# Kernel tuning notes

Hardware: AMD Instinct MI355X
Metric: run time of the kernel (lower is better)

The kernel has to match this reference:

```python
import jax, jax.numpy as jnp
import numpy as np

N_NODES = 50000
N_EDGES = 800000
N_GRAPHS = 64
IN_DIM = 128
HID = 32
HEADS = 4
EDGE_DIM = 8
OUT = 10


def setup_inputs() -> dict:
    key = jax.random.key(0)
    ks = jax.random.split(key, 20)
    s = 0.1
    inp = {
        "x": jax.random.normal(ks[0], (N_NODES, IN_DIM), jnp.float32),
        "edge_index": jax.random.randint(ks[1], (2, N_EDGES), 0, N_NODES, jnp.int32),
        "edge_attr": jax.random.normal(ks[2], (N_EDGES, EDGE_DIM), jnp.float32),
        "batch": jnp.sort(jax.random.randint(ks[3], (N_NODES,), 0, N_GRAPHS, jnp.int32)),
        # conv1: heads=4, out=32
        "W1": jax.random.normal(ks[4], (IN_DIM, HEADS * HID), jnp.float32) * s,
        "att_src1": jax.random.normal(ks[5], (HEADS, HID), jnp.float32) * s,
        "att_dst1": jax.random.normal(ks[6], (HEADS, HID), jnp.float32) * s,
        "We1": jax.random.normal(ks[7], (EDGE_DIM, HEADS * HID), jnp.float32) * s,
        "att_e1": jax.random.normal(ks[8], (HEADS, HID), jnp.float32) * s,
        "b1": jnp.zeros((HEADS * HID,), jnp.float32),
        # conv2: heads=1, out=32
        "W2": jax.random.normal(ks[9], (HEADS * HID, HID), jnp.float32) * s,
        "att_src2": jax.random.normal(ks[10], (1, HID), jnp.float32) * s,
        "att_dst2": jax.random.normal(ks[11], (1, HID), jnp.float32) * s,
        "We2": jax.random.normal(ks[12], (EDGE_DIM, HID), jnp.float32) * s,
        "att_e2": jax.random.normal(ks[13], (1, HID), jnp.float32) * s,
        "b2": jnp.zeros((HID,), jnp.float32),
        # MLP head
        "W3": jax.random.normal(ks[14], (HID, HID // 2), jnp.float32) * s,
        "b3": jnp.zeros((HID // 2,), jnp.float32),
        "W4": jax.random.normal(ks[15], (HID // 2, OUT), jnp.float32) * s,
        "b4": jnp.zeros((OUT,), jnp.float32),
    }
    return inp


def _gat_conv(x, src, dst, eattr, W, a_s, a_d, We, a_e, b, H, C, N):
    """PyG GATConv math (self-loops already appended to src/dst/eattr)."""
    h = (x @ W).reshape(-1, H, C)            # [N,H,C]
    e = (eattr @ We).reshape(-1, H, C)       # [E,H,C]
    al_s = jnp.sum(h * a_s, -1)              # [N,H]
    al_d = jnp.sum(h * a_d, -1)              # [N,H]
    alpha = al_s[src] + al_d[dst] + jnp.sum(e * a_e, -1)   # [E,H]
    alpha = jax.nn.leaky_relu(alpha, 0.2)
    # segment softmax over incoming edges of each dst node
    m = jax.ops.segment_max(alpha, dst, num_segments=N)
    ealpha = jnp.exp(alpha - m[dst])
    denom = jax.ops.segment_sum(ealpha, dst, num_segments=N)
    ealpha = ealpha / (denom[dst] + 1e-16)
    msg = h[src] * ealpha[:, :, None]        # [E,H,C]
    out = jax.ops.segment_sum(msg, dst, num_segments=N)  # [N,H,C]
    return out.reshape(N, H * C) + b


def _forward(x, edge_index, edge_attr, batch,
             W1, att_src1, att_dst1, We1, att_e1, b1,
             W2, att_src2, att_dst2, We2, att_e2, b2,
             W3, b3, W4, b4):
    N = x.shape[0]
    src, dst = edge_index[0], edge_index[1]
    # add_self_loops with fill_value='mean': loop attr = mean of incoming edge_attr
    cnt = jax.ops.segment_sum(jnp.ones((src.shape[0],), x.dtype), dst, num_segments=N)
    loop_attr = jax.ops.segment_sum(edge_attr, dst, num_segments=N) / jnp.maximum(cnt, 1.0)[:, None]
    ar = jnp.arange(N, dtype=src.dtype)
    src2 = jnp.concatenate([src, ar])
    dst2 = jnp.concatenate([dst, ar])
    eattr2 = jnp.concatenate([edge_attr, loop_attr], axis=0)

    h = _gat_conv(x, src2, dst2, eattr2, W1, att_src1, att_dst1, We1, att_e1, b1, HEADS, HID, N)
    h = jax.nn.elu(h)
    h = _gat_conv(h, src2, dst2, eattr2, W2, att_src2, att_dst2, We2, att_e2, b2, 1, HID, N)
    h = jax.nn.elu(h)
    # global mean pool per graph
    gsum = jax.ops.segment_sum(h, batch, num_segments=N_GRAPHS)
    gcnt = jax.ops.segment_sum(jnp.ones((N,), h.dtype), batch, num_segments=N_GRAPHS)
    g = gsum / jnp.maximum(gcnt, 1.0)[:, None]
    # MLP head (eval mode: dropout is identity)
    z = jax.nn.relu(g @ W3 + b3)
    return z @ W4 + b4


def reference(x, edge_index, edge_attr, batch,
              W1, att_src1, att_dst1, We1, att_e1, b1,
              W2, att_src2, att_dst2, We2, att_e2, b2,
              W3, b3, W4, b4):
    return _forward(x, edge_index, edge_attr, batch,
                    W1, att_src1, att_dst1, We1, att_e1, b1,
                    W2, att_src2, att_dst2, We2, att_e2, b2,
                    W3, b3, W4, b4)
```

## Files before the change

### kernel.cpp

```cpp
#include <hip/hip_runtime.h>
#include <hip/hip_bf16.h>
#include <math.h>

#define N_NODES 50000
#define N_EDGES 800000
#define N_GRAPHS 64
#define IN_DIM 128
#define HID 32
#define HEADS 4
#define EDGE_DIM 8
#define OUT_DIM 10
#define HC 128
#define NB 196
#define G1H 782

__device__ __forceinline__ float leaky(float x){ return x >= 0.f ? x : 0.2f*x; }
__device__ __forceinline__ float elu_f(float x){ return x > 0.f ? x : __expf(x)-1.f; }

__device__ __forceinline__ float bf2f(unsigned short u){
  union { unsigned int i; float f; } v; v.i = ((unsigned int)u) << 16; return v.f;
}
__device__ __forceinline__ float lo16(unsigned int u){
  union { unsigned int i; float f; } v; v.i = u << 16; return v.f;
}
__device__ __forceinline__ float hi16(unsigned int u){
  union { unsigned int i; float f; } v; v.i = u & 0xffff0000u; return v.f;
}
__device__ __forceinline__ unsigned short f2bf(float f){
  union { float f; unsigned int i; } v; v.f = f;
  unsigned int r = v.i + 0x7FFF + ((v.i >> 16) & 1);
  return (unsigned short)(r >> 16);
}

__device__ __forceinline__ void gemm1_body(int bb, float* xs, float* ws,
    const float* __restrict__ x, const float* __restrict__ W1,
    const float* __restrict__ as1, const float* __restrict__ ad1,
    unsigned short* __restrict__ h1b, float* __restrict__ als1, float* __restrict__ ald1){
  int t = threadIdx.x;
  int cg = t & 15, c8 = cg*8, qb = (t >> 4)*2;
  int base = bb * 32;
  for (int i = t; i < 1024; i += 256){
    int node = base + (i >> 5);
    int col = (i & 31) * 4;
    float4 v = make_float4(0,0,0,0);
    if (node < N_NODES) v = *(const float4*)&x[node*IN_DIM + col];
    *(float4*)&xs[(i>>5)*128 + col] = v;
  }
  float acc[2][8];
  #pragma unroll
  for (int q = 0; q < 2; q++)
    #pragma unroll
    for (int i = 0; i < 8; i++) acc[q][i] = 0.f;

  for (int kb = 0; kb < 128; kb += 32){
    __syncthreads();
    for (int i = t; i < 1024; i += 256)
      *(float4*)&ws[i*4] = *(const float4*)&W1[kb*128 + i*4];
    __syncthreads();
    #pragma unroll 8
    for (int k = 0; k < 32; k++){
      float4 w0 = *(float4*)&ws[k*128 + c8];
      float4 w1 = *(float4*)&ws[k*128 + c8 + 4];
      #pragma unroll
      for (int q = 0; q < 2; q++){
        float xv = xs[(qb + q)*128 + kb + k];
        acc[q][0] = fmaf(xv, w0.x, acc[q][0]);
        acc[q][1] = fmaf(xv, w0.y, acc[q][1]);
        acc[q][2] = fmaf(xv, w0.z, acc[q][2]);
        acc[q][3] = fmaf(xv, w0.w, acc[q][3]);
        acc[q][4] = fmaf(xv, w1.x, acc[q][4]);
        acc[q][5] = fmaf(xv, w1.y, acc[q][5]);
        acc[q][6] = fmaf(xv, w1.z, acc[q][6]);
        acc[q][7] = fmaf(xv, w1.w, acc[q][7]);
      }
    }
  }
  int head = cg >> 2;
  float asv[8], adv[8];
  #pragma unroll
  for (int i = 0; i < 8; i++){ asv[i] = as1[c8 + i]; adv[i] = ad1[c8 + i]; }
  #pragma unroll
  for (int q = 0; q < 2; q++){
    int n = base + qb + q;
    if (n >= N_NODES) continue;
    float sa = 0.f, sd = 0.f;
    #pragma unroll
    for (int i = 0; i < 8; i++){
      sa = fmaf(acc[q][i], asv[i], sa);
      sd = fmaf(acc[q][i], adv[i], sd);
    }
    sa += __shfl_xor(sa, 1); sd += __shfl_xor(sd, 1);
    sa += __shfl_xor(sa, 2); sd += __shfl_xor(sd, 2);
    uint4 pk;
    pk.x = (unsigned int)f2bf(acc[q][0]) | ((unsigned int)f2bf(acc[q][1]) << 16);
    pk.y = (unsigned int)f2bf(acc[q][2]) | ((unsigned int)f2bf(acc[q][3]) << 16);
    pk.z = (unsigned int)f2bf(acc[q][4]) | ((unsigned int)f2bf(acc[q][5]) << 16);
    pk.w = (unsigned int)f2bf(acc[q][6]) | ((unsigned int)f2bf(acc[q][7]) << 16);
    *(uint4*)&h1b[n*HC + c8] = pk;
    if ((cg & 3) == 0){ als1[n*4 + head] = sa; ald1[n*4 + head] = sd; }
  }
}

__global__ __launch_bounds__(256) void k_f1(const int* __restrict__ dst, int* __restrict__ cnt,
    int* __restrict__ rank,
    const float* __restrict__ x, const float* __restrict__ W1,
    const float* __restrict__ as1, const float* __restrict__ ad1,
    unsigned short* __restrict__ h1b, float* __restrict__ als1, float* __restrict__ ald1){
  __shared__ float smem[8192];
  int m = blockIdx.x % 5, r = blockIdx.x / 5;
  if (m < 4){
    int e = (r*4 + m)*256 + threadIdx.x;
    if (e < N_EDGES) rank[e] = atomicAdd(&cnt[dst[e]], 1);
    return;
  }
  gemm1_body(r, smem, smem + 4096, x, W1, as1, ad1, h1b, als1, ald1);
}

__global__ __launch_bounds__(256) void k_blocksum(const int* __restrict__ cnt, int* __restrict__ bsum){
  __shared__ int sh[256];
  int n = blockIdx.x*256 + threadIdx.x;
  sh[threadIdx.x] = (n < N_NODES) ? cnt[n] : 0;
  __syncthreads();
  for (int off = 128; off > 0; off >>= 1){
    if (threadIdx.x < off) sh[threadIdx.x] += sh[threadIdx.x + off];
    __syncthreads();
  }
  if (threadIdx.x == 0) bsum[blockIdx.x] = sh[0];
}

__global__ __launch_bounds__(256) void k_scanb(const int* __restrict__ bsum, int* __restrict__ bpre){
  __shared__ int sh[256];
  int t = threadIdx.x;
  int v = (t < NB) ? bsum[t] : 0;
  sh[t] = v; __syncthreads();
  for (int off = 1; off < 256; off <<= 1){
    int u = (t >= off) ? sh[t-off] : 0;
    __syncthreads();
    sh[t] += u;
    __syncthreads();
  }
  if (t < NB) bpre[t] = sh[t] - v;
}

__global__ __launch_bounds__(256) void k_rowptr(const int* __restrict__ cnt, const int* __restrict__ bpre,
    int* __restrict__ rowptr){
  __shared__ int sh[256];
  int t = threadIdx.x; int n = blockIdx.x*256 + t;
  int c = (n < N_NODES) ? cnt[n] : 0;
  sh[t] = c; __syncthreads();
  for (int off = 1; off < 256; off <<= 1){
    int u = (t >= off) ? sh[t-off] : 0;
    __syncthreads();
    sh[t] += u;
    __syncthreads();
  }
  int incl = sh[t];
  if (n < N_NODES){
    rowptr[n] = bpre[blockIdx.x] + incl - c;
  }
  if (n == N_NODES-1) rowptr[N_NODES] = bpre[blockIdx.x] + incl;
}

__global__ __launch_bounds__(256) void k_f2(const int* __restrict__ src, const int* __restrict__ dst,
    const int* __restrict__ rank, const int* __restrict__ rowptr,
    const float* __restrict__ eattr,
    const float* __restrict__ We1, const float* __restrict__ ae1w,
    const float* __restrict__ We2, const float* __restrict__ ae2w,
    int4* __restrict__ rec,
    const float* __restrict__ x, const float* __restrict__ W1,
    const float* __restrict__ as1, const float* __restrict__ ad1,
    unsigned short* __restrict__ h1b, float* __restrict__ als1, float* __restrict__ ald1){
  __shared__ float smem[8192];
  int m = blockIdx.x % 5, r = blockIdx.x / 5;
  if (m < 4){
    int t = threadIdx.x;
    if (t < 32){
      int d = t >> 2, h = t & 3;
      float s = 0.f;
      for (int c = 0; c < 32; c++) s = fmaf(We1[d*128 + h*32 + c], ae1w[h*32 + c], s);
      smem[d*4 + h] = s;
    } else if (t < 40){
      int d = t - 32;
      float s = 0.f;
      for (int c = 0; c < 32; c++) s = fmaf(We2[d*32 + c], ae2w[c], s);
      smem[32 + d] = s;
    }
    __syncthreads();
    int e = (r*4 + m)*256 + t;
    if (e >= N_EDGES) return;
    int sv = src[e], d = dst[e], rk = rank[e];
    float4 x0 = *(const float4*)&eattr[e*8];
    float4 x1 = *(const float4*)&eattr[e*8+4];
    int pos = rowptr[d] + rk;
    float ea[8] = {x0.x,x0.y,x0.z,x0.w,x1.x,x1.y,x1.z,x1.w};
    float4 rr = make_float4(0,0,0,0);
    float r2 = 0.f;
    #pragma unroll
    for (int dd = 0; dd < 8; dd++){
      rr.x = fmaf(ea[dd], smem[dd*4+0], rr.x);
      rr.y = fmaf(ea[dd], smem[dd*4+1], rr.y);
      rr.z = fmaf(ea[dd], smem[dd*4+2], rr.z);
      rr.w = fmaf(ea[dd], smem[dd*4+3], rr.w);
      r2   = fmaf(ea[dd], smem[32+dd], r2);
    }
    int4 rv;
    rv.x = sv;
    rv.y = (int)((unsigned int)f2bf(rr.x) | ((unsigned int)f2bf(rr.y) << 16));
    rv.z = (int)((unsigned int)f2bf(rr.z) | ((unsigned int)f2bf(rr.w) << 16));
    rv.w = __float_as_int(r2);
    rec[pos] = rv;
    return;
  }
  gemm1_body(G1H + r, smem, smem + 4096, x, W1, as1, ad1, h1b, als1, ald1);
}

__global__ __launch_bounds__(256) void k_conv1(const int* __restrict__ rowptr, const int4* __restrict__ rec,
    const float* __restrict__ als1, const float* __restrict__ ald1,
    const unsigned short* __restrict__ h1b, const float* __restrict__ b1,
    unsigned short* __restrict__ heb){
  int wv = threadIdx.x >> 6, l = threadIdx.x & 63;
  int n = blockIdx.x*4 + wv;
  if (n >= N_NODES) return;
  int g = l >> 4, il = l & 15;
  int c0 = il*8, h = il >> 2;
  int hs1 = (h & 1) * 16;
  float ad = ald1[n*4 + h];
  float den = 0.f, sum_ae = 0.f;
  float acc[8];
  #pragma unroll
  for (int i = 0; i < 8; i++) acc[i] = 0.f;
  int r0 = rowptr[n], r1 = rowptr[n+1];
  for (int k = r0 + g; k < r1; k += 4){
    int4 q = rec[k];
    unsigned int w = (h & 2) ? (unsigned int)q.z : (unsigned int)q.y;
    float aev = bf2f((unsigned short)(w >> hs1));
    float as_v = als1[q.x*4 + h];
    uint4 hv = *(const uint4*)(h1b + q.x*HC + c0);
    float p = __expf(leaky(as_v + ad + aev));
    sum_ae += aev; den += p;
    acc[0] = fmaf(p, lo16(hv.x), acc[0]);
    acc[1] = fmaf(p, hi16(hv.x), acc[1]);
    acc[2] = fmaf(p, lo16(hv.y), acc[2]);
    acc[3] = fmaf(p, hi16(hv.y), acc[3]);
    acc[4] = fmaf(p, lo16(hv.z), acc[4]);
    acc[5] = fmaf(p, hi16(hv.z), acc[5]);
    acc[6] = fmaf(p, lo16(hv.w), acc[6]);
    acc[7] = fmaf(p, hi16(hv.w), acc[7]);
  }
  #pragma unroll
  for (int off = 16; off < 64; off <<= 1){
    den    += __shfl_xor(den, off);
    sum_ae += __shfl_xor(sum_ae, off);
    #pragma unroll
    for (int i = 0; i < 8; i++) acc[i] += __shfl_xor(acc[i], off);
  }
  int cn = r1 - r0; if (cn < 1) cn = 1;
  float ps = __expf(leaky(als1[n*4 + h] + ad + sum_ae / (float)cn));
  uint4 hs = *(const uint4*)(h1b + n*HC + c0);
  den += ps;
  acc[0] = fmaf(ps, lo16(hs.x), acc[0]);
  acc[1] = fmaf(ps, hi16(hs.x), acc[1]);
  acc[2] = fmaf(ps, lo16(hs.y), acc[2]);
  acc[3] = fmaf(ps, hi16(hs.y), acc[3]);
  acc[4] = fmaf(ps, lo16(hs.z), acc[4]);
  acc[5] = fmaf(ps, hi16(hs.z), acc[5]);
  acc[6] = fmaf(ps, lo16(hs.w), acc[6]);
  acc[7] = fmaf(ps, hi16(hs.w), acc[7]);
  float inv = 1.f / (den + 1e-16f);
  float4 bv0 = *(const float4*)&b1[c0];
  float4 bv1 = *(const float4*)&b1[c0 + 4];
  float o0 = elu_f(fmaf(acc[0], inv, bv0.x));
  float o1 = elu_f(fmaf(acc[1], inv, bv0.y));
  float o2 = elu_f(fmaf(acc[2], inv, bv0.z));
  float o3 = elu_f(fmaf(acc[3], inv, bv0.w));
  float o4 = elu_f(fmaf(acc[4], inv, bv1.x));
  float o5 = elu_f(fmaf(acc[5], inv, bv1.y));
  float o6 = elu_f(fmaf(acc[6], inv, bv1.z));
  float o7 = elu_f(fmaf(acc[7], inv, bv1.w));
  if (g == 0){
    uint4 pk;
    pk.x = (unsigned int)f2bf(o0) | ((unsigned int)f2bf(o1) << 16);
    pk.y = (unsigned int)f2bf(o2) | ((unsigned int)f2bf(o3) << 16);
    pk.z = (unsigned int)f2bf(o4) | ((unsigned int)f2bf(o5) << 16);
    pk.w = (unsigned int)f2bf(o6) | ((unsigned int)f2bf(o7) << 16);
    *(uint4*)(heb + n*HC + c0) = pk;
  }
}

__global__ __launch_bounds__(256) void k_gemm2(const unsigned short* __restrict__ heb,
    const float* __restrict__ W2, const float* __restrict__ as2, const float* __restrict__ ad2,
    unsigned short* __restrict__ h2b, float* __restrict__ als2, float* __restrict__ ald2){
  __shared__ float ws[128*32];
  __shared__ float xs[16][128];
  int t = threadIdx.x; int c = t & 31; int j = t >> 5;
  int base = blockIdx.x * 16;
  for (int i = t; i < 1024; i += 256)
    *(float4*)&ws[i*4] = *(const float4*)&W2[i*4];
  {
    int node = base + (t >> 4);
    int col = (t & 15) * 8;
    uint4 v = make_uint4(0,0,0,0);
    if (node < N_NODES) v = *(const uint4*)(heb + node*128 + col);
    float* xp = &xs[t>>4][col];
    xp[0] = bf2f((unsigned short)v.x); xp[1] = bf2f((unsigned short)(v.x>>16));
    xp[2] = bf2f((unsigned short)v.y); xp[3] = bf2f((unsigned short)(v.y>>16));
    xp[4] = bf2f((unsigned short)v.z); xp[5] = bf2f((unsigned short)(v.z>>16));
    xp[6] = bf2f((unsigned short)v.w); xp[7] = bf2f((unsigned short)(v.w>>16));
  }
  __syncthreads();
  float s0 = 0.f, s1 = 0.f;
  #pragma unroll 8
  for (int k = 0; k < 128; k++){
    float w = ws[k*32 + c];
    s0 = fmaf(xs[j*2][k],   w, s0);
    s1 = fmaf(xs[j*2+1][k], w, s1);
  }
  float a2c = as2[c], d2c = ad2[c];
  int n0 = base + j*2, n1 = n0 + 1;
  float sa0 = s0*a2c, sd0 = s0*d2c, sa1 = s1*a2c, sd1 = s1*d2c;
  #pragma unroll
  for (int off = 1; off < 32; off <<= 1){
    sa0 += __shfl_xor(sa0, off); sd0 += __shfl_xor(sd0, off);
    sa1 += __shfl_xor(sa1, off); sd1 += __shfl_xor(sd1, off);
  }
  if (n0 < N_NODES){ h2b[n0*32 + c] = f2bf(s0); if (c == 0){ als2[n0] = sa0; ald2[n0] = sd0; } }
  if (n1 < N_NODES){ h2b[n1*32 + c] = f2bf(s1); if (c == 0){ als2[n1] = sa1; ald2[n1] = sd1; } }
}

__global__ __launch_bounds__(256) void k_conv2(const int* __restrict__ rowptr, const int4* __restrict__ rec,
    const float* __restrict__ als2, const float* __restrict__ ald2,
    const unsigned short* __restrict__ h2b, const float* __restrict__ b2, float* __restrict__ out2){
  int wv = threadIdx.x >> 6, l = threadIdx.x & 63;
  int n = blockIdx.x*4 + wv;
  if (n >= N_NODES) return;
  int g = l >> 3, il = l & 7;
  int c0 = il*4;
  float ad = ald2[n];
  float den = 0.f, sum_ae = 0.f;
  float acc[4];
  #pragma unroll
  for (int i = 0; i < 4; i++) acc[i] = 0.f;
  int r0 = rowptr[n], r1 = rowptr[n+1];
  for (int k = r0 + g; k < r1; k += 8){
    int4 q = rec[k];
    float aev = __int_as_float(q.w);
    float as_v = als2[q.x];
    uint2 hv = *(const uint2*)(h2b + q.x*32 + c0);
    float p = __expf(leaky(as_v + ad + aev));
    sum_ae += aev; den += p;
    acc[0] = fmaf(p, lo16(hv.x), acc[0]);
    acc[1] = fmaf(p, hi16(hv.x), acc[1]);
    acc[2] = fmaf(p, lo16(hv.y), acc[2]);
    acc[3] = fmaf(p, hi16(hv.y), acc[3]);
  }
  #pragma unroll
  for (int off = 8; off < 64; off <<= 1){
    den    += __shfl_xor(den, off);
    sum_ae += __shfl_xor(sum_ae, off);
    #pragma unroll
    for (int i = 0; i < 4; i++) acc[i] += __shfl_xor(acc[i], off);
  }
  int cn = r1 - r0; if (cn < 1) cn = 1;
  float ps = __expf(leaky(als2[n] + ad + sum_ae / (float)cn));
  uint2 hs = *(const uint2*)(h2b + n*32 + c0);
  den += ps;
  acc[0] = fmaf(ps, lo16(hs.x), acc[0]);
  acc[1] = fmaf(ps, hi16(hs.x), acc[1]);
  acc[2] = fmaf(ps, lo16(hs.y), acc[2]);
  acc[3] = fmaf(ps, hi16(hs.y), acc[3]);
  float inv = 1.f / (den + 1e-16f);
  float4 bv = *(const float4*)&b2[c0];
  if (g == 0){
    float4 ov;
    ov.x = elu_f(fmaf(acc[0], inv, bv.x));
    ov.y = elu_f(fmaf(acc[1], inv, bv.y));
    ov.z = elu_f(fmaf(acc[2], inv, bv.z));
    ov.w = elu_f(fmaf(acc[3], inv, bv.w));
    *(float4*)&out2[n*32 + c0] = ov;
  }
}

__global__ __launch_bounds__(256) void k_pool(const float* __restrict__ out2, const int* __restrict__ batch,
    float* __restrict__ gpool){
  int g = blockIdx.x;
  int a = 0, b = N_NODES;
  while (a < b){ int mid = (a + b) >> 1; if (batch[mid] < g) a = mid + 1; else b = mid; }
  int lo = a;
  a = lo; b = N_NODES;
  while (a < b){ int mid = (a + b) >> 1; if (batch[mid] < g + 1) a = mid + 1; else b = mid; }
  int hi = a;
  int t = threadIdx.x, c = t & 31, r = t >> 5;
  float s = 0.f;
  for (int n = lo + r; n < hi; n += 8) s += out2[n*32 + c];
  __shared__ float sh[256];
  sh[t] = s; __syncthreads();
  if (r == 0){
    for (int q = 1; q < 8; q++) s += sh[q*32 + c];
    int cg = hi - lo; if (cg < 1) cg = 1;
    gpool[g*32 + c] = s / (float)cg;
  }
}

__global__ __launch_bounds__(1024) void k_mlp(const float* __restrict__ gpool, const float* __restrict__ W3,
    const float* __restrict__ b3, const float* __restrict__ W4, const float* __restrict__ b4,
    float* __restrict__ out){
  __shared__ float z[64*16];
  int t = threadIdx.x;
  {
    int g = t >> 4, jj = t & 15;
    float s = b3[jj];
    #pragma unroll
    for (int c = 0; c < 32; c++) s = fmaf(gpool[g*32 + c], W3[c*16 + jj], s);
    z[t] = fmaxf(s, 0.f);
  }
  __syncthreads();
  if (t < 640){
    int g = t / 10, o = t - g*10;
    float s = b4[o];
    #pragma unroll
    for (int jj = 0; jj < 16; jj++) s = fmaf(z[g*16 + jj], W4[jj*10 + o], s);
    out[t] = s;
  }
}

extern "C" void kernel_launch(void* const* d_in, const int* in_sizes, int n_in,
                              void* d_out, int out_size, void* d_ws, size_t ws_size,
                              hipStream_t stream) {
  (void)in_sizes; (void)n_in; (void)out_size; (void)ws_size;
  const float* x     = (const float*)d_in[0];
  const int*   ei    = (const int*)  d_in[1];
  const float* eattr = (const float*)d_in[2];
  const int*   batch = (const int*)  d_in[3];
  const float* W1    = (const float*)d_in[4];
  const float* as1   = (const float*)d_in[5];
  const float* ad1   = (const float*)d_in[6];
  const float* We1   = (const float*)d_in[7];
  const float* ae1w  = (const float*)d_in[8];
  const float* b1    = (const float*)d_in[9];
  const float* W2    = (const float*)d_in[10];
  const float* as2   = (const float*)d_in[11];
  const float* ad2   = (const float*)d_in[12];
  const float* We2   = (const float*)d_in[13];
  const float* ae2w  = (const float*)d_in[14];
  const float* b2    = (const float*)d_in[15];
  const float* W3    = (const float*)d_in[16];
  const float* b3    = (const float*)d_in[17];
  const float* W4    = (const float*)d_in[18];
  const float* b4    = (const float*)d_in[19];
  float* out = (float*)d_out;
  const int* src  = ei;
  const int* dstp = ei + N_EDGES;

  char* p = (char*)d_ws;
  auto alloc = [&](size_t bytes)->void*{ void* r = (void*)p; p += (bytes + 255) & ~(size_t)255; return r; };
  int*    cnt      = (int*)   alloc(4*N_NODES);
  size_t  zero_bytes = (size_t)(p - (char*)d_ws);
  int*    rank     = (int*)   alloc(4*N_EDGES);
  int*    rowptr   = (int*)   alloc(4*(N_NODES+1));
  int*    bsum     = (int*)   alloc(4*NB);
  int*    bpre     = (int*)   alloc(4*NB);
  int4*   rec      = (int4*)  alloc(16*N_EDGES);
  unsigned short* h1b  = (unsigned short*)alloc(2*N_NODES*HC);
  float*  als1     = (float*) alloc(16*N_NODES);
  float*  ald1     = (float*) alloc(16*N_NODES);
  unsigned short* heb  = (unsigned short*)alloc(2*N_NODES*HC);
  unsigned short* h2b  = (unsigned short*)alloc(2*N_NODES*HID);
  float*  als2     = (float*) alloc(4*N_NODES);
  float*  ald2     = (float*) alloc(4*N_NODES);
  float*  out2     = (float*) alloc(4*N_NODES*HID);
  float*  gpool    = (float*) alloc(4*N_GRAPHS*HID);

  const int FGRID = G1H * 5;

  hipMemsetAsync(d_ws, 0, zero_bytes, stream);
  k_f1      <<<FGRID, 256, 0, stream>>>(dstp, cnt, rank, x, W1, as1, ad1, h1b, als1, ald1);
  k_blocksum<<<NB,    256, 0, stream>>>(cnt, bsum);
  k_scanb   <<<1,     256, 0, stream>>>(bsum, bpre);
  k_rowptr  <<<NB,    256, 0, stream>>>(cnt, bpre, rowptr);
  k_f2      <<<FGRID, 256, 0, stream>>>(src, dstp, rank, rowptr, eattr, We1, ae1w, We2, ae2w,
                                        rec, x, W1, as1, ad1, h1b, als1, ald1);
  k_conv1   <<<(N_NODES+3)/4, 256, 0, stream>>>(rowptr, rec, als1, ald1, h1b, b1, heb);
  k_gemm2   <<<(N_NODES+15)/16, 256, 0, stream>>>(heb, W2, as2, ad2, h2b, als2, ald2);
  k_conv2   <<<(N_NODES+3)/4, 256, 0, stream>>>(rowptr, rec, als2, ald2, h2b, b2, out2);
  k_pool    <<<N_GRAPHS, 256, 0, stream>>>(out2, batch, gpool);
  k_mlp     <<<1,    1024, 0, stream>>>(gpool, W3, b3, W4, b4, out);
}
```

Before: 345.0 us.

## Replace global atomic CSR build with LDS-privatized chunked histogram and scatter

New measurement: 349.3 us. About the same (+1.3%).

```diff
diff --git a/kernel.cpp b/kernel.cpp
--- a/kernel.cpp
+++ b/kernel.cpp
@@ -13,6 +13,13 @@
 #define HC 128
 #define NB 196
 #define G1H 782
+#define G1TOT 1563
+#define CH 128
+#define EPC 6250
+#define RQ 4
+#define RNG 12500
+#define NBH 512
+#define KGRID 1305
 
 __device__ __forceinline__ float leaky(float x){ return x >= 0.f ? x : 0.2f*x; }
 __device__ __forceinline__ float elu_f(float x){ return x > 0.f ? x : __expf(x)-1.f; }
@@ -101,19 +108,49 @@
   }
 }
 
-__global__ __launch_bounds__(256) void k_f1(const int* __restrict__ dst, int* __restrict__ cnt,
-    int* __restrict__ rank,
+__global__ __launch_bounds__(256) void k_hist(const int* __restrict__ dst,
+    unsigned short* __restrict__ part,
     const float* __restrict__ x, const float* __restrict__ W1,
     const float* __restrict__ as1, const float* __restrict__ ad1,
     unsigned short* __restrict__ h1b, float* __restrict__ als1, float* __restrict__ ald1){
-  __shared__ float smem[8192];
+  __shared__ unsigned int ldsU[12544];
   int m = blockIdx.x % 5, r = blockIdx.x / 5;
-  if (m < 4){
-    int e = (r*4 + m)*256 + threadIdx.x;
-    if (e < N_EDGES) rank[e] = atomicAdd(&cnt[dst[e]], 1);
+  int t = threadIdx.x;
+  if (m < 2){
+    int hb = r*2 + m;
+    if (hb >= NBH) return;
+    int c = hb >> 2, rg = hb & 3;
+    int lo = rg * RNG;
+    for (int i = t; i < RNG; i += 256) ldsU[i] = 0;
+    __syncthreads();
+    int e0 = c * EPC;
+    for (int i = t; i < EPC; i += 256){
+      int d = dst[e0 + i];
+      unsigned int dr = (unsigned int)(d - lo);
+      if (dr < RNG) atomicAdd(&ldsU[dr], 1u);
+    }
+    __syncthreads();
+    for (int i = t; i < RNG; i += 256)
+      part[(size_t)c*N_NODES + lo + i] = (unsigned short)ldsU[i];
     return;
   }
-  gemm1_body(r, smem, smem + 4096, x, W1, as1, ad1, h1b, als1, ald1);
+  int gb = r*3 + (m-2);
+  if (gb >= G1H) return;
+  gemm1_body(gb, (float*)ldsU, (float*)ldsU + 4096, x, W1, as1, ad1, h1b, als1, ald1);
+}
+
+__global__ __launch_bounds__(256) void k_cprefix(unsigned short* __restrict__ part,
+    int* __restrict__ cnt){
+  int n = blockIdx.x*256 + threadIdx.x;
+  if (n >= N_NODES) return;
+  unsigned int run = 0;
+  for (int c = 0; c < CH; c++){
+    size_t idx = (size_t)c*N_NODES + n;
+    unsigned int v = part[idx];
+    part[idx] = (unsigned short)run;
+    run += v;
+  }
+  cnt[n] = (int)run;
 }
 
 __global__ __launch_bounds__(256) void k_blocksum(const int* __restrict__ cnt, int* __restrict__ bsum){
@@ -161,8 +198,8 @@
   if (n == N_NODES-1) rowptr[N_NODES] = bpre[blockIdx.x] + incl;
 }
 
-__global__ __launch_bounds__(256) void k_f2(const int* __restrict__ src, const int* __restrict__ dst,
-    const int* __restrict__ rank, const int* __restrict__ rowptr,
+__global__ __launch_bounds__(256) void k_scat(const int* __restrict__ src, const int* __restrict__ dst,
+    const unsigned short* __restrict__ part, const int* __restrict__ rowptr,
     const float* __restrict__ eattr,
     const float* __restrict__ We1, const float* __restrict__ ae1w,
     const float* __restrict__ We2, const float* __restrict__ ae2w,
@@ -170,48 +207,64 @@
     const float* __restrict__ x, const float* __restrict__ W1,
     const float* __restrict__ as1, const float* __restrict__ ad1,
     unsigned short* __restrict__ h1b, float* __restrict__ als1, float* __restrict__ ald1){
-  __shared__ float smem[8192];
+  __shared__ unsigned int ldsU[12544];
+  __shared__ float wproj[40];
   int m = blockIdx.x % 5, r = blockIdx.x / 5;
-  if (m < 4){
-    int t = threadIdx.x;
+  int t = threadIdx.x;
+  if (m < 2){
+    int sb = r*2 + m;
+    if (sb >= NBH) return;
+    int c = sb >> 2, rg = sb & 3;
+    int lo = rg * RNG;
     if (t < 32){
       int d = t >> 2, h = t & 3;
       float s = 0.f;
-      for (int c = 0; c < 32; c++) s = fmaf(We1[d*128 + h*32 + c], ae1w[h*32 + c], s);
-      smem[d*4 + h] = s;
+      for (int cc = 0; cc < 32; cc++) s = fmaf(We1[d*128 + h*32 + cc], ae1w[h*32 + cc], s);
+      wproj[d*4 + h] = s;
     } else if (t < 40){
       int d = t - 32;
       float s = 0.f;
-      for (int c = 0; c < 32; c++) s = fmaf(We2[d*32 + c], ae2w[c], s);
-      smem[32 + d] = s;
+      for (int cc = 0; cc < 32; cc++) s = fmaf(We2[d*32 + cc], ae2w[cc], s);
+      wproj[32 + d] = s;
     }
-    __syncthreads();
-    int e = (r*4 + m)*256 + t;
-    if (e >= N_EDGES) return;
-    int sv = src[e], d = dst[e], rk = rank[e];
-    float4 x0 = *(const float4*)&eattr[e*8];
-    float4 x1 = *(const float4*)&eattr[e*8+4];
-    int pos = rowptr[d] + rk;
-    float ea[8] = {x0.x,x0.y,x0.z,x0.w,x1.x,x1.y,x1.z,x1.w};
-    float4 rr = make_float4(0,0,0,0);
-    float r2 = 0.f;
-    #pragma unroll
-    for (int dd = 0; dd < 8; dd++){
-      rr.x = fmaf(ea[dd], smem[dd*4+0], rr.x);
-      rr.y = fmaf(ea[dd], smem[dd*4+1], rr.y);
-      rr.z = fmaf(ea[dd], smem[dd*4+2], rr.z);
-      rr.w = fmaf(ea[dd], smem[dd*4+3], rr.w);
-      r2   = fmaf(ea[dd], smem[32+dd], r2);
+    for (int i = t; i < RNG; i += 256)
+      ldsU[i] = (unsigned int)part[(size_t)c*N_NODES + lo + i];
+    __syncthreads();
+    int e0 = c * EPC;
+    for (int i = t; i < EPC; i += 256){
+      int e = e0 + i;
+      int d = dst[e];
+      unsigned int dr = (unsigned int)(d - lo);
+      if (dr < RNG){
+        int sv = src[e];
+        float4 x0 = *(const float4*)&eattr[(size_t)e*8];
+        float4 x1 = *(const float4*)&eattr[(size_t)e*8 + 4];
+        float ea[8] = {x0.x,x0.y,x0.z,x0.w,x1.x,x1.y,x1.z,x1.w};
+        float4 rr = make_float4(0,0,0,0);
+        float r2 = 0.f;
+        #pragma unroll
+        for (int dd = 0; dd < 8; dd++){
+          rr.x = fmaf(ea[dd], wproj[dd*4+0], rr.x);
+          rr.y = fmaf(ea[dd], wproj[dd*4+1], rr.y);
+          rr.z = fmaf(ea[dd], wproj[dd*4+2], rr.z);
+          rr.w = fmaf(ea[dd], wproj[dd*4+3], rr.w);
+          r2   = fmaf(ea[dd], wproj[32+dd], r2);
+        }
+        unsigned int lr = atomicAdd(&ldsU[dr], 1u);
+        int pos = rowptr[d] + (int)lr;
+        int4 rv;
+        rv.x = sv;
+        rv.y = (int)((unsigned int)f2bf(rr.x) | ((unsigned int)f2bf(rr.y) << 16));
+        rv.z = (int)((unsigned int)f2bf(rr.z) | ((unsigned int)f2bf(rr.w) << 16));
+        rv.w = __float_as_int(r2);
+        rec[pos] = rv;
+      }
     }
-    int4 rv;
-    rv.x = sv;
-    rv.y = (int)((unsigned int)f2bf(rr.x) | ((unsigned int)f2bf(rr.y) << 16));
-    rv.z = (int)((unsigned int)f2bf(rr.z) | ((unsigned int)f2bf(rr.w) << 16));
-    rv.w = __float_as_int(r2);
-    rec[pos] = rv;
     return;
   }
-  gemm1_body(G1H + r, smem, smem + 4096, x, W1, as1, ad1, h1b, als1, ald1);
+  int gb = G1H + r*3 + (m-2);
+  if (gb >= G1TOT) return;
+  gemm1_body(gb, (float*)ldsU, (float*)ldsU + 4096, x, W1, as1, ad1, h1b, als1, ald1);
 }
 
 __global__ __launch_bounds__(256) void k_conv1(const int* __restrict__ rowptr, const int4* __restrict__ rec,
@@ -454,8 +507,6 @@
   char* p = (char*)d_ws;
   auto alloc = [&](size_t bytes)->void*{ void* r = (void*)p; p += (bytes + 255) & ~(size_t)255; return r; };
   int*    cnt      = (int*)   alloc(4*N_NODES);
-  size_t  zero_bytes = (size_t)(p - (char*)d_ws);
-  int*    rank     = (int*)   alloc(4*N_EDGES);
   int*    rowptr   = (int*)   alloc(4*(N_NODES+1));
   int*    bsum     = (int*)   alloc(4*NB);
   int*    bpre     = (int*)   alloc(4*NB);
@@ -469,15 +520,14 @@
   float*  ald2     = (float*) alloc(4*N_NODES);
   float*  out2     = (float*) alloc(4*N_NODES*HID);
   float*  gpool    = (float*) alloc(4*N_GRAPHS*HID);
-
-  const int FGRID = G1H * 5;
-
-  hipMemsetAsync(d_ws, 0, zero_bytes, stream);
-  k_f1      <<<FGRID, 256, 0, stream>>>(dstp, cnt, rank, x, W1, as1, ad1, h1b, als1, ald1);
+  unsigned short* part = heb;
+
+  k_hist    <<<KGRID, 256, 0, stream>>>(dstp, part, x, W1, as1, ad1, h1b, als1, ald1);
+  k_cprefix <<<NB,    256, 0, stream>>>(part, cnt);
   k_blocksum<<<NB,    256, 0, stream>>>(cnt, bsum);
   k_scanb   <<<1,     256, 0, stream>>>(bsum, bpre);
   k_rowptr  <<<NB,    256, 0, stream>>>(cnt, bpre, rowptr);
-  k_f2      <<<FGRID, 256, 0, stream>>>(src, dstp, rank, rowptr, eattr, We1, ae1w, We2, ae2w,
+  k_scat    <<<KGRID, 256, 0, stream>>>(src, dstp, part, rowptr, eattr, We1, ae1w, We2, ae2w,
                                         rec, x, W1, as1, ad1, h1b, als1, ald1);
   k_conv1   <<<(N_NODES+3)/4, 256, 0, stream>>>(rowptr, rec, als1, ald1, h1b, b1, heb);
   k_gemm2   <<<(N_NODES+15)/16, 256, 0, stream>>>(heb, W2, as2, ad2, h2b, als2, ald2);
```

## Fuse conv1 output with layer-2 GEMM and move all GEMM1 into first kernel

Applied to the files above, without the earlier changes.

New measurement: 333.5 us. 1.03x faster.

```diff
diff --git a/kernel.cpp b/kernel.cpp
--- a/kernel.cpp
+++ b/kernel.cpp
@@ -12,7 +12,9 @@
 #define OUT_DIM 10
 #define HC 128
 #define NB 196
-#define G1H 782
+#define G1TOT 1563
+#define K1GRID 4689
+#define EBLK 3125
 
 __device__ __forceinline__ float leaky(float x){ return x >= 0.f ? x : 0.2f*x; }
 __device__ __forceinline__ float elu_f(float x){ return x > 0.f ? x : __expf(x)-1.f; }
@@ -107,9 +109,9 @@
     const float* __restrict__ as1, const float* __restrict__ ad1,
     unsigned short* __restrict__ h1b, float* __restrict__ als1, float* __restrict__ ald1){
   __shared__ float smem[8192];
-  int m = blockIdx.x % 5, r = blockIdx.x / 5;
-  if (m < 4){
-    int e = (r*4 + m)*256 + threadIdx.x;
+  int m = blockIdx.x % 3, r = blockIdx.x / 3;
+  if (m < 2){
+    int e = (r*2 + m)*256 + threadIdx.x;
     if (e < N_EDGES) rank[e] = atomicAdd(&cnt[dst[e]], 1);
     return;
   }
@@ -166,61 +168,54 @@
     const float* __restrict__ eattr,
     const float* __restrict__ We1, const float* __restrict__ ae1w,
     const float* __restrict__ We2, const float* __restrict__ ae2w,
-    int4* __restrict__ rec,
-    const float* __restrict__ x, const float* __restrict__ W1,
-    const float* __restrict__ as1, const float* __restrict__ ad1,
-    unsigned short* __restrict__ h1b, float* __restrict__ als1, float* __restrict__ ald1){
-  __shared__ float smem[8192];
-  int m = blockIdx.x % 5, r = blockIdx.x / 5;
-  if (m < 4){
-    int t = threadIdx.x;
-    if (t < 32){
-      int d = t >> 2, h = t & 3;
-      float s = 0.f;
-      for (int c = 0; c < 32; c++) s = fmaf(We1[d*128 + h*32 + c], ae1w[h*32 + c], s);
-      smem[d*4 + h] = s;
-    } else if (t < 40){
-      int d = t - 32;
-      float s = 0.f;
-      for (int c = 0; c < 32; c++) s = fmaf(We2[d*32 + c], ae2w[c], s);
-      smem[32 + d] = s;
-    }
-    __syncthreads();
-    int e = (r*4 + m)*256 + t;
-    if (e >= N_EDGES) return;
-    int sv = src[e], d = dst[e], rk = rank[e];
-    float4 x0 = *(const float4*)&eattr[e*8];
-    float4 x1 = *(const float4*)&eattr[e*8+4];
-    int pos = rowptr[d] + rk;
-    float ea[8] = {x0.x,x0.y,x0.z,x0.w,x1.x,x1.y,x1.z,x1.w};
-    float4 rr = make_float4(0,0,0,0);
-    float r2 = 0.f;
-    #pragma unroll
-    for (int dd = 0; dd < 8; dd++){
-      rr.x = fmaf(ea[dd], smem[dd*4+0], rr.x);
-      rr.y = fmaf(ea[dd], smem[dd*4+1], rr.y);
-      rr.z = fmaf(ea[dd], smem[dd*4+2], rr.z);
-      rr.w = fmaf(ea[dd], smem[dd*4+3], rr.w);
-      r2   = fmaf(ea[dd], smem[32+dd], r2);
-    }
-    int4 rv;
-    rv.x = sv;
-    rv.y = (int)((unsigned int)f2bf(rr.x) | ((unsigned int)f2bf(rr.y) << 16));
-    rv.z = (int)((unsigned int)f2bf(rr.z) | ((unsigned int)f2bf(rr.w) << 16));
-    rv.w = __float_as_int(r2);
-    rec[pos] = rv;
-    return;
-  }
-  gemm1_body(G1H + r, smem, smem + 4096, x, W1, as1, ad1, h1b, als1, ald1);
+    int4* __restrict__ rec){
+  __shared__ float wproj[40];
+  int t = threadIdx.x;
+  if (t < 32){
+    int d = t >> 2, h = t & 3;
+    float s = 0.f;
+    for (int c = 0; c < 32; c++) s = fmaf(We1[d*128 + h*32 + c], ae1w[h*32 + c], s);
+    wproj[d*4 + h] = s;
+  } else if (t < 40){
+    int d = t - 32;
+    float s = 0.f;
+    for (int c = 0; c < 32; c++) s = fmaf(We2[d*32 + c], ae2w[c], s);
+    wproj[32 + d] = s;
+  }
+  __syncthreads();
+  int e = blockIdx.x*256 + t;
+  if (e >= N_EDGES) return;
+  int sv = src[e], d = dst[e], rk = rank[e];
+  float4 x0 = *(const float4*)&eattr[(size_t)e*8];
+  float4 x1 = *(const float4*)&eattr[(size_t)e*8 + 4];
+  int pos = rowptr[d] + rk;
+  float ea[8] = {x0.x,x0.y,x0.z,x0.w,x1.x,x1.y,x1.z,x1.w};
+  float4 rr = make_float4(0,0,0,0);
+  float r2 = 0.f;
+  #pragma unroll
+  for (int dd = 0; dd < 8; dd++){
+    rr.x = fmaf(ea[dd], wproj[dd*4+0], rr.x);
+    rr.y = fmaf(ea[dd], wproj[dd*4+1], rr.y);
+    rr.z = fmaf(ea[dd], wproj[dd*4+2], rr.z);
+    rr.w = fmaf(ea[dd], wproj[dd*4+3], rr.w);
+    r2   = fmaf(ea[dd], wproj[32+dd], r2);
+  }
+  int4 rv;
+  rv.x = sv;
+  rv.y = (int)((unsigned int)f2bf(rr.x) | ((unsigned int)f2bf(rr.y) << 16));
+  rv.z = (int)((unsigned int)f2bf(rr.z) | ((unsigned int)f2bf(rr.w) << 16));
+  rv.w = __float_as_int(r2);
+  rec[pos] = rv;
 }
 
 __global__ __launch_bounds__(256) void k_conv1(const int* __restrict__ rowptr, const int4* __restrict__ rec,
     const float* __restrict__ als1, const float* __restrict__ ald1,
     const unsigned short* __restrict__ h1b, const float* __restrict__ b1,
-    unsigned short* __restrict__ heb){
+    const float* __restrict__ W2, const float* __restrict__ as2, const float* __restrict__ ad2,
+    unsigned short* __restrict__ h2b, float* __restrict__ als2, float* __restrict__ ald2){
+  __shared__ float oex[4][128];
   int wv = threadIdx.x >> 6, l = threadIdx.x & 63;
   int n = blockIdx.x*4 + wv;
-  if (n >= N_NODES) return;
   int g = l >> 4, il = l & 15;
   int c0 = il*8, h = il >> 2;
   int hs1 = (h & 1) * 16;
@@ -277,54 +272,26 @@
   float o5 = elu_f(fmaf(acc[5], inv, bv1.y));
   float o6 = elu_f(fmaf(acc[6], inv, bv1.z));
   float o7 = elu_f(fmaf(acc[7], inv, bv1.w));
+  float* op = oex[wv];
   if (g == 0){
-    uint4 pk;
-    pk.x = (unsigned int)f2bf(o0) | ((unsigned int)f2bf(o1) << 16);
-    pk.y = (unsigned int)f2bf(o2) | ((unsigned int)f2bf(o3) << 16);
-    pk.z = (unsigned int)f2bf(o4) | ((unsigned int)f2bf(o5) << 16);
-    pk.w = (unsigned int)f2bf(o6) | ((unsigned int)f2bf(o7) << 16);
-    *(uint4*)(heb + n*HC + c0) = pk;
-  }
-}
-
-__global__ __launch_bounds__(256) void k_gemm2(const unsigned short* __restrict__ heb,
-    const float* __restrict__ W2, const float* __restrict__ as2, const float* __restrict__ ad2,
-    unsigned short* __restrict__ h2b, float* __restrict__ als2, float* __restrict__ ald2){
-  __shared__ float ws[128*32];
-  __shared__ float xs[16][128];
-  int t = threadIdx.x; int c = t & 31; int j = t >> 5;
-  int base = blockIdx.x * 16;
-  for (int i = t; i < 1024; i += 256)
-    *(float4*)&ws[i*4] = *(const float4*)&W2[i*4];
-  {
-    int node = base + (t >> 4);
-    int col = (t & 15) * 8;
-    uint4 v = make_uint4(0,0,0,0);
-    if (node < N_NODES) v = *(const uint4*)(heb + node*128 + col);
-    float* xp = &xs[t>>4][col];
-    xp[0] = bf2f((unsigned short)v.x); xp[1] = bf2f((unsigned short)(v.x>>16));
-    xp[2] = bf2f((unsigned short)v.y); xp[3] = bf2f((unsigned short)(v.y>>16));
-    xp[4] = bf2f((unsigned short)v.z); xp[5] = bf2f((unsigned short)(v.z>>16));
-    xp[6] = bf2f((unsigned short)v.w); xp[7] = bf2f((unsigned short)(v.w>>16));
+    *(float4*)&op[c0]     = make_float4(o0, o1, o2, o3);
+    *(float4*)&op[c0 + 4] = make_float4(o4, o5, o6, o7);
   }
   __syncthreads();
-  float s0 = 0.f, s1 = 0.f;
+  int j = l & 31, hf = l >> 5;
+  int cb = hf * 64;
+  float s = 0.f;
   #pragma unroll 8
-  for (int k = 0; k < 128; k++){
-    float w = ws[k*32 + c];
-    s0 = fmaf(xs[j*2][k],   w, s0);
-    s1 = fmaf(xs[j*2+1][k], w, s1);
-  }
-  float a2c = as2[c], d2c = ad2[c];
-  int n0 = base + j*2, n1 = n0 + 1;
-  float sa0 = s0*a2c, sd0 = s0*d2c, sa1 = s1*a2c, sd1 = s1*d2c;
+  for (int c = 0; c < 64; c++)
+    s = fmaf(op[cb + c], W2[(cb + c)*32 + j], s);
+  s += __shfl_xor(s, 32);
+  float sa = s * as2[j], sd = s * ad2[j];
   #pragma unroll
   for (int off = 1; off < 32; off <<= 1){
-    sa0 += __shfl_xor(sa0, off); sd0 += __shfl_xor(sd0, off);
-    sa1 += __shfl_xor(sa1, off); sd1 += __shfl_xor(sd1, off);
-  }
-  if (n0 < N_NODES){ h2b[n0*32 + c] = f2bf(s0); if (c == 0){ als2[n0] = sa0; ald2[n0] = sd0; } }
-  if (n1 < N_NODES){ h2b[n1*32 + c] = f2bf(s1); if (c == 0){ als2[n1] = sa1; ald2[n1] = sd1; } }
+    sa += __shfl_xor(sa, off); sd += __shfl_xor(sd, off);
+  }
+  if (l < 32) h2b[n*32 + j] = f2bf(s);
+  if (l == 0){ als2[n] = sa; ald2[n] = sd; }
 }
 
 __global__ __launch_bounds__(256) void k_conv2(const int* __restrict__ rowptr, const int4* __restrict__ rec,
@@ -463,24 +430,20 @@
   unsigned short* h1b  = (unsigned short*)alloc(2*N_NODES*HC);
   float*  als1     = (float*) alloc(16*N_NODES);
   float*  ald1     = (float*) alloc(16*N_NODES);
-  unsigned short* heb  = (unsigned short*)alloc(2*N_NODES*HC);
   unsigned short* h2b  = (unsigned short*)alloc(2*N_NODES*HID);
   float*  als2     = (float*) alloc(4*N_NODES);
   float*  ald2     = (float*) alloc(4*N_NODES);
   float*  out2     = (float*) alloc(4*N_NODES*HID);
   float*  gpool    = (float*) alloc(4*N_GRAPHS*HID);
 
-  const int FGRID = G1H * 5;
-
   hipMemsetAsync(d_ws, 0, zero_bytes, stream);
-  k_f1      <<<FGRID, 256, 0, stream>>>(dstp, cnt, rank, x, W1, as1, ad1, h1b, als1, ald1);
+  k_f1      <<<K1GRID, 256, 0, stream>>>(dstp, cnt, rank, x, W1, as1, ad1, h1b, als1, ald1);
   k_blocksum<<<NB,    256, 0, stream>>>(cnt, bsum);
   k_scanb   <<<1,     256, 0, stream>>>(bsum, bpre);
   k_rowptr  <<<NB,    256, 0, stream>>>(cnt, bpre, rowptr);
-  k_f2      <<<FGRID, 256, 0, stream>>>(src, dstp, rank, rowptr, eattr, We1, ae1w, We2, ae2w,
-                                        rec, x, W1, as1, ad1, h1b, als1, ald1);
-  k_conv1   <<<(N_NODES+3)/4, 256, 0, stream>>>(rowptr, rec, als1, ald1, h1b, b1, heb);
-  k_gemm2   <<<(N_NODES+15)/16, 256, 0, stream>>>(heb, W2, as2, ad2, h2b, als2, ald2);
+  k_f2      <<<EBLK,  256, 0, stream>>>(src, dstp, rank, rowptr, eattr, We1, ae1w, We2, ae2w, rec);
+  k_conv1   <<<N_NODES/4, 256, 0, stream>>>(rowptr, rec, als1, ald1, h1b, b1,
+                                            W2, as2, ad2, h2b, als2, ald2);
   k_conv2   <<<(N_NODES+3)/4, 256, 0, stream>>>(rowptr, rec, als2, ald2, h2b, b2, out2);
   k_pool    <<<N_GRAPHS, 256, 0, stream>>>(out2, batch, gpool);
   k_mlp     <<<1,    1024, 0, stream>>>(gpool, W3, b3, W4, b4, out);
```
